# Kernel optimization log

Measured on AMD Instinct MI355X. Metric: run time of the kernel, lower is better.

The kernel has to match this reference:

```python
import jax, jax.numpy as jnp
import numpy as np

NUM_HEADS = 12
HEAD_SIZE = 64
HIDDEN = NUM_HEADS * HEAD_SIZE  # 768
ONE_SIDED_WINDOW = 256          # attention_window 512 // 2
NEG = -10000.0


def setup_inputs() -> dict:
    key = jax.random.key(0)
    ks = jax.random.split(key, 16)
    B, W, E, H = 1, 2048, 128, HIDDEN
    std = 0.02
    def lin(kw, kb):
        return (jax.random.normal(kw, (H, H), jnp.float32) * std,
                jax.random.normal(kb, (H,), jnp.float32) * std)
    q_w, q_b = lin(ks[0], ks[1])
    k_w, k_b = lin(ks[2], ks[3])
    v_w, v_b = lin(ks[4], ks[5])
    w2e_w, w2e_b = lin(ks[6], ks[7])
    e2w_w, e2w_b = lin(ks[8], ks[9])
    e2e_w, e2e_b = lin(ks[10], ks[11])
    return {
        "word_hidden_states": jax.random.normal(ks[12], (B, W, H), jnp.float32),
        "entity_hidden_states": jax.random.normal(ks[13], (B, E, H), jnp.float32),
        "attention_mask": jnp.zeros((B, 1, 1, W + E), jnp.float32),
        "q_w": q_w, "q_b": q_b, "k_w": k_w, "k_b": k_b, "v_w": v_w, "v_b": v_b,
        "w2e_w": w2e_w, "w2e_b": w2e_b, "e2w_w": e2w_w, "e2w_b": e2w_b,
        "e2e_w": e2e_w, "e2e_b": e2e_b,
    }


def reference(word_hidden_states, entity_hidden_states, attention_mask,
              q_w, q_b, k_w, k_b, v_w, v_b,
              w2e_w, w2e_b, e2w_w, e2w_b, e2e_w, e2e_b):
    B, W, H = word_hidden_states.shape
    E = entity_hidden_states.shape[1]
    S = W + E

    def heads(x):  # [B, L, H] -> [B, nh, L, hd]
        return x.reshape(B, -1, NUM_HEADS, HEAD_SIZE).transpose(0, 2, 1, 3)

    concat = jnp.concatenate([word_hidden_states, entity_hidden_states], axis=1)
    k = heads(concat @ k_w + k_b)          # [B, nh, S, hd]
    v = heads(concat @ v_w + v_b)
    q_w2w = heads(word_hidden_states @ q_w + q_b)
    q_w2e = heads(word_hidden_states @ w2e_w + w2e_b)
    q_e2w = heads(entity_hidden_states @ e2w_w + e2w_b)
    q_e2e = heads(entity_hidden_states @ e2e_w + e2e_b)

    k_word, k_ent = k[:, :, :W], k[:, :, W:]

    # --- w2w: Longformer sliding-window QK^T, then _conversion to a dense
    # [B, nh, W, W] matrix with out-of-band entries set to -10000. ---
    w2w = jnp.einsum('bhid,bhjd->bhij', q_w2w, k_word)  # [B, nh, W, W]
    idx = jnp.arange(W)
    in_band = jnp.abs(idx[:, None] - idx[None, :]) <= ONE_SIDED_WINDOW  # [W, W]
    # diagonal mask: float_mask[j] (-10000 where attention_mask != 0) added
    # within the band (broadcast over heads / query positions)
    mask_words = attention_mask[:, 0, 0, :W]                # [B, W]
    float_mask = jnp.where(mask_words != 0.0, NEG, 0.0)     # [B, W]
    w2w = w2w + float_mask[:, None, None, :]
    # _conversion: out-of-band -> -10000; also exact zeros -> -10000 (source quirk)
    w2w = jnp.where(in_band[None, None] & (w2w != 0.0), w2w, NEG)

    # --- entity-aware dense blocks ---
    w2e = jnp.einsum('bhid,bhjd->bhij', q_w2e, k_ent)    # [B, nh, W, E]
    e2w = jnp.einsum('bhid,bhjd->bhij', q_e2w, k_word)   # [B, nh, E, W]
    e2e = jnp.einsum('bhid,bhjd->bhij', q_e2e, k_ent)    # [B, nh, E, E]

    word_scores = jnp.concatenate([w2w, w2e], axis=3)    # [B, nh, W, S]
    ent_scores = jnp.concatenate([e2w, e2e], axis=3)     # [B, nh, E, S]
    scores = jnp.concatenate([word_scores, ent_scores], axis=2)  # [B, nh, S, S]

    scores = scores / jnp.sqrt(jnp.float32(HEAD_SIZE)) + attention_mask
    probs = jax.nn.softmax(scores, axis=-1)

    ctx = jnp.einsum('bhij,bhjd->bhid', probs, v)        # [B, nh, S, hd]
    ctx = ctx.transpose(0, 2, 1, 3).reshape(B, S, H)
    return ctx[:, :W, :], ctx[:, W:, :]
```

## Files before the change

### kernel.cpp

```cpp
#include <hip/hip_runtime.h>

typedef __bf16 bf16x8 __attribute__((ext_vector_type(8)));
typedef unsigned short u16x8 __attribute__((ext_vector_type(8)));
typedef u16x8 u16x8_a __attribute__((may_alias));
typedef unsigned int u32x4 __attribute__((ext_vector_type(4)));
typedef u32x4 u32x4_a __attribute__((may_alias));
typedef float f32x4 __attribute__((ext_vector_type(4)));

#define LOG2E 1.4426950408889634f
#define NEGV  -10000.0f

__device__ __forceinline__ float bf2f(unsigned short u){
  union{unsigned int i; float f;} x; x.i = ((unsigned int)u)<<16; return x.f;
}
__device__ __forceinline__ unsigned short f2bf(float f){
  union{float f; unsigned int i;} x; x.f=f;
  unsigned int i = x.i;
  return (unsigned short)((i + 0x7FFFu + ((i>>16)&1u)) >> 16);
}
__device__ __forceinline__ u16x8 cvt8(float4 a, float4 b){
  u16x8 r;
  r[0]=f2bf(a.x); r[1]=f2bf(a.y); r[2]=f2bf(a.z); r[3]=f2bf(a.w);
  r[4]=f2bf(b.x); r[5]=f2bf(b.y); r[6]=f2bf(b.z); r[7]=f2bf(b.w);
  return r;
}
__device__ __forceinline__ bf16x8 ldb(const unsigned short* p){
  return __builtin_bit_cast(bf16x8, *(const u16x8_a*)p);
}

__global__ __launch_bounds__(256) void transpose6(
    const float* __restrict__ w0, const float* __restrict__ w1,
    const float* __restrict__ w2, const float* __restrict__ w3,
    const float* __restrict__ w4, const float* __restrict__ w5,
    unsigned short* __restrict__ outT)
{
  const float* src;
  switch (blockIdx.z){
    case 0: src = w0; break; case 1: src = w1; break; case 2: src = w2; break;
    case 3: src = w3; break; case 4: src = w4; break; default: src = w5; break;
  }
  unsigned short* dst = outT + (size_t)blockIdx.z * 589824;
  __shared__ float tile[32][33];
  int tx = threadIdx.x, ty = threadIdx.y;
  int x0 = blockIdx.x*32, y0 = blockIdx.y*32;
  #pragma unroll
  for (int i=0;i<32;i+=8) tile[ty+i][tx] = src[(size_t)(y0+ty+i)*768 + x0+tx];
  __syncthreads();
  #pragma unroll
  for (int i=0;i<32;i+=8) dst[(size_t)(x0+ty+i)*768 + y0+tx] = f2bf(tile[tx][ty+i]);
}

__global__ __launch_bounds__(256) void transpose_v(
    const unsigned short* __restrict__ Vb, unsigned short* __restrict__ VbT)
{
  __shared__ unsigned short t[32][33];
  int tx = threadIdx.x, ty = threadIdx.y;
  int x0 = blockIdx.x*32;
  int y0 = blockIdx.y*32;
  #pragma unroll
  for (int i=0;i<32;i+=8) t[ty+i][tx] = Vb[(size_t)(x0+ty+i)*768 + y0+tx];
  __syncthreads();
  #pragma unroll
  for (int i=0;i<32;i+=8) VbT[(size_t)(y0+ty+i)*2176 + x0+tx] = t[tx][ty+i];
}

__global__ __launch_bounds__(256) void gemm_proj(
    const float* __restrict__ word, const float* __restrict__ ent,
    const unsigned short* __restrict__ wT,
    const float* __restrict__ bK, const float* __restrict__ bV,
    const float* __restrict__ bQ, const float* __restrict__ bWE,
    const float* __restrict__ bEW, const float* __restrict__ bEE,
    unsigned short* __restrict__ oK, unsigned short* __restrict__ oV,
    unsigned short* __restrict__ oQ, unsigned short* __restrict__ oWE,
    unsigned short* __restrict__ oEW, unsigned short* __restrict__ oEE)
{
  int mt = blockIdx.x, ntile = blockIdx.y;
  int g, mg;
  if      (mt < 17){ g=0; mg=mt;    }
  else if (mt < 34){ g=1; mg=mt-17; }
  else if (mt < 50){ g=2; mg=mt-34; }
  else if (mt < 66){ g=3; mg=mt-50; }
  else if (mt < 67){ g=4; mg=0;     }
  else             { g=5; mg=0;     }
  int m0 = mg*128;
  const float* A;
  if (g<=1)      A = (mg<16) ? (word + (size_t)m0*768) : ent;
  else if (g<=3) A = word + (size_t)m0*768;
  else           A = ent;
  const unsigned short* B = wT + (size_t)g*589824;
  const float* bias; unsigned short* out;
  switch (g){
    case 0: bias=bK;  out=oK;  break;
    case 1: bias=bV;  out=oV;  break;
    case 2: bias=bQ;  out=oQ;  break;
    case 3: bias=bWE; out=oWE; break;
    case 4: bias=bEW; out=oEW; break;
    default:bias=bEE; out=oEE; break;
  }
  out += (size_t)m0*768;
  int n0 = ntile*128;

  __shared__ __align__(16) unsigned short a_s[128*32];
  __shared__ __align__(16) unsigned short b_s[128*32];

  int tid  = threadIdx.x;
  int w    = tid>>6, lane = tid&63, quad = lane>>4, lr = lane&15;
  int wm   = (w&1)*64, wn = (w>>1)*64;

  f32x4 acc[4][4];
  #pragma unroll
  for (int i=0;i<4;i++) for (int j=0;j<4;j++) for (int r=0;r<4;r++) acc[i][j][r]=0.f;

  int ar = tid>>1;
  int ak = (tid&1)*16;
  const float* Arow = A + (size_t)ar*768 + ak;
  const unsigned short* Brow = B + (size_t)(n0+ar)*768 + ak;

  for (int k0=0; k0<768; k0+=32){
    float4 af0 = *(const float4*)(Arow + k0);
    float4 af1 = *(const float4*)(Arow + k0 + 4);
    float4 af2 = *(const float4*)(Arow + k0 + 8);
    float4 af3 = *(const float4*)(Arow + k0 + 12);
    u16x8 av0 = cvt8(af0, af1);
    u16x8 av1 = cvt8(af2, af3);
    u16x8 bv0 = *(const u16x8_a*)(Brow + k0);
    u16x8 bv1 = *(const u16x8_a*)(Brow + k0 + 8);
    __syncthreads();
    *(u16x8_a*)(a_s + ar*32 + ak)     = av0;
    *(u16x8_a*)(a_s + ar*32 + ak + 8) = av1;
    *(u16x8_a*)(b_s + ar*32 + ak)     = bv0;
    *(u16x8_a*)(b_s + ar*32 + ak + 8) = bv1;
    __syncthreads();
    bf16x8 af[4], bfr[4];
    #pragma unroll
    for (int i=0;i<4;i++) af[i]  = ldb(a_s + (wm+i*16+lr)*32 + quad*8);
    #pragma unroll
    for (int i=0;i<4;i++) bfr[i] = ldb(b_s + (wn+i*16+lr)*32 + quad*8);
    #pragma unroll
    for (int i=0;i<4;i++)
      #pragma unroll
      for (int j=0;j<4;j++)
        acc[i][j] = __builtin_amdgcn_mfma_f32_16x16x32_bf16(af[i], bfr[j], acc[i][j], 0,0,0);
  }
  #pragma unroll
  for (int j=0;j<4;j++){
    int col = n0 + wn + j*16 + lr;
    float bb = bias[col];
    #pragma unroll
    for (int i=0;i<4;i++){
      int rowb = wm + i*16 + quad*4;
      #pragma unroll
      for (int r=0;r<4;r++)
        out[(size_t)(rowb+r)*768 + col] = f2bf(acc[i][j][r] + bb);
    }
  }
}

__global__ __launch_bounds__(256) void attn_split(
  const unsigned short* __restrict__ Kb,  const unsigned short* __restrict__ VbT,
  const unsigned short* __restrict__ Qw,  const unsigned short* __restrict__ Qwe,
  const unsigned short* __restrict__ Qew, const unsigned short* __restrict__ Qee,
  const float* __restrict__ am,
  float* __restrict__ outw, float* __restrict__ oute)
{
  int bx = blockIdx.x, h = blockIdx.y;
  int tid = threadIdx.x, w = tid>>6, lane = tid&63, quad = lane>>4, lr = lane&15;
  bool isword = bx < 64;
  int qrb, kh, nsplit;
  const unsigned short *Qa, *Qb;
  float* outp;
  if (isword){ qrb = bx*32 + (w>>1)*16; kh = w&1; nsplit = 2; Qa=Qw;  Qb=Qwe; outp=outw; }
  else       { qrb = (bx-64)*16;        kh = w;   nsplit = 4; Qa=Qew; Qb=Qee; outp=oute; }

  __shared__ __align__(16) unsigned int p32[4][16*24];
  __shared__ float mrg[4][64][24];

  const unsigned short* qr = Qa + (size_t)(qrb+lr)*768 + h*64 + quad*8;
  bf16x8 qa0 = ldb(qr), qa1 = ldb(qr + 32);
  qr = Qb + (size_t)(qrb+lr)*768 + h*64 + quad*8;
  bf16x8 qb0 = ldb(qr), qb1 = ldb(qr + 32);

  float m_r[4], l_r[4];
  f32x4 o[4];
  #pragma unroll
  for (int r=0;r<4;r++){ m_r[r] = -1e30f; l_r[r] = 0.f; }
  #pragma unroll
  for (int n2=0;n2<4;n2++) for (int r=0;r<4;r++) o[n2][r] = 0.f;

  int lo, nw;
  if (isword){
    lo = qrb - 256; if (lo < 0) lo = 0; lo &= ~31;
    int hi = qrb + 272; if (hi > 2048) hi = 2048; hi = (hi + 31) & ~31;
    nw = (hi - lo) >> 5;
  } else { lo = 0; nw = 64; }
  int nc = nw + 4;

  for (int c = kh; c < nc; c += nsplit){
    bool entp = c >= nw;
    int j0 = entp ? (2048 + (c-nw)*32) : (lo + c*32);

    const unsigned short* kp = Kb + (size_t)(j0+lr)*768 + h*64 + quad*8;
    bf16x8 k00 = ldb(kp),          k01 = ldb(kp + 32);
    bf16x8 k10 = ldb(kp + 16*768), k11 = ldb(kp + 16*768 + 32);
    const unsigned short* vp = VbT + (size_t)(h*64 + lr)*2176 + j0 + quad*8;
    bf16x8 v0 = ldb(vp), v1 = ldb(vp + 16*2176), v2 = ldb(vp + 32*2176), v3 = ldb(vp + 48*2176);

    bf16x8 qf0 = entp ? qb0 : qa0;
    bf16x8 qf1 = entp ? qb1 : qa1;
    f32x4 s[2];
    {
      f32x4 z0 = {0.f,0.f,0.f,0.f}, z1 = {0.f,0.f,0.f,0.f};
      z0 = __builtin_amdgcn_mfma_f32_16x16x32_bf16(qf0, k00, z0, 0,0,0);
      z0 = __builtin_amdgcn_mfma_f32_16x16x32_bf16(qf1, k01, z0, 0,0,0);
      z1 = __builtin_amdgcn_mfma_f32_16x16x32_bf16(qf0, k10, z1, 0,0,0);
      z1 = __builtin_amdgcn_mfma_f32_16x16x32_bf16(qf1, k11, z1, 0,0,0);
      s[0] = z0; s[1] = z1;
    }

    float sc[2][4];
    bool wband = isword && !entp;
    #pragma unroll
    for (int t=0;t<2;t++){
      int j = j0 + t*16 + lr;
      float amj  = am[j];
      float addl = amj * LOG2E;
      #pragma unroll
      for (int r=0;r<4;r++){
        float sv = s[t][r];
        if (wband){
          sv += (amj != 0.f) ? NEGV : 0.f;
          int i = qrb + quad*4 + r;
          bool ok = ((unsigned)(i - j + 256) <= 512u) && (sv != 0.f);
          sv = ok ? sv : NEGV;
        }
        sc[t][r] = sv * (LOG2E*0.125f) + addl;
      }
    }

    #pragma unroll
    for (int r=0;r<4;r++){
      float mx = fmaxf(sc[0][r], sc[1][r]);
      mx = fmaxf(mx, __shfl_xor(mx, 1));
      mx = fmaxf(mx, __shfl_xor(mx, 2));
      mx = fmaxf(mx, __shfl_xor(mx, 4));
      mx = fmaxf(mx, __shfl_xor(mx, 8));
      float mn = fmaxf(m_r[r], mx);
      float alpha = exp2f(m_r[r] - mn);
      m_r[r] = mn;
      float p0 = exp2f(sc[0][r]-mn), p1 = exp2f(sc[1][r]-mn);
      unsigned short pb0 = f2bf(p0), pb1 = f2bf(p1);
      float rs = bf2f(pb0) + bf2f(pb1);
      rs += __shfl_xor(rs,1); rs += __shfl_xor(rs,2);
      rs += __shfl_xor(rs,4); rs += __shfl_xor(rs,8);
      l_r[r] = l_r[r]*alpha + rs;
      p32[w][(quad*4+r)*24 + lr] = (unsigned int)pb0 | ((unsigned int)pb1 << 16);
      #pragma unroll
      for (int n2=0;n2<4;n2++) o[n2][r] *= alpha;
    }

    const unsigned int* pbp = &p32[w][lr*24 + (quad&1)*8];
    u32x4 ra = *(const u32x4_a*)pbp;
    u32x4 rb = *(const u32x4_a*)(pbp + 4);
    unsigned int pf32[4];
    if (quad < 2){
      pf32[0] = (ra[0]&0xFFFFu) | (ra[1]<<16);
      pf32[1] = (ra[2]&0xFFFFu) | (ra[3]<<16);
      pf32[2] = (rb[0]&0xFFFFu) | (rb[1]<<16);
      pf32[3] = (rb[2]&0xFFFFu) | (rb[3]<<16);
    } else {
      pf32[0] = (ra[0]>>16) | (ra[1]&0xFFFF0000u);
      pf32[1] = (ra[2]>>16) | (ra[3]&0xFFFF0000u);
      pf32[2] = (rb[0]>>16) | (rb[1]&0xFFFF0000u);
      pf32[3] = (rb[2]>>16) | (rb[3]&0xFFFF0000u);
    }
    u32x4 pfv = {pf32[0], pf32[1], pf32[2], pf32[3]};
    bf16x8 pf = __builtin_bit_cast(bf16x8, pfv);

    o[0] = __builtin_amdgcn_mfma_f32_16x16x32_bf16(pf, v0, o[0], 0,0,0);
    o[1] = __builtin_amdgcn_mfma_f32_16x16x32_bf16(pf, v1, o[1], 0,0,0);
    o[2] = __builtin_amdgcn_mfma_f32_16x16x32_bf16(pf, v2, o[2], 0,0,0);
    o[3] = __builtin_amdgcn_mfma_f32_16x16x32_bf16(pf, v3, o[3], 0,0,0);
  }

  {
    float* my = &mrg[w][lane][0];
    #pragma unroll
    for (int r=0;r<4;r++){ my[r] = m_r[r]; my[4+r] = l_r[r]; }
    #pragma unroll
    for (int n2=0;n2<4;n2++)
      #pragma unroll
      for (int r=0;r<4;r++) my[8+n2*4+r] = o[n2][r];
  }
  __syncthreads();
  if (kh == 0){
    for (int p=1; p<nsplit; p++){
      const float* pr = &mrg[w+p][lane][0];
      #pragma unroll
      for (int r=0;r<4;r++){
        float m2 = pr[r], l2 = pr[4+r];
        float M  = fmaxf(m_r[r], m2);
        float e1 = exp2f(m_r[r]-M), e2 = exp2f(m2-M);
        m_r[r] = M;
        l_r[r] = l_r[r]*e1 + l2*e2;
        #pragma unroll
        for (int n2=0;n2<4;n2++)
          o[n2][r] = o[n2][r]*e1 + pr[8+n2*4+r]*e2;
      }
    }
    #pragma unroll
    for (int n2=0;n2<4;n2++)
      #pragma unroll
      for (int r=0;r<4;r++){
        int row = qrb + quad*4 + r;
        outp[(size_t)row*768 + h*64 + n2*16 + lr] = o[n2][r] / l_r[r];
      }
  }
}

extern "C" void kernel_launch(void* const* d_in, const int* in_sizes, int n_in,
                              void* d_out, int out_size, void* d_ws, size_t ws_size,
                              hipStream_t stream) {
  const float* word  = (const float*)d_in[0];
  const float* ent   = (const float*)d_in[1];
  const float* am    = (const float*)d_in[2];
  const float* q_w   = (const float*)d_in[3];
  const float* q_b   = (const float*)d_in[4];
  const float* k_w   = (const float*)d_in[5];
  const float* k_b   = (const float*)d_in[6];
  const float* v_w   = (const float*)d_in[7];
  const float* v_b   = (const float*)d_in[8];
  const float* w2e_w = (const float*)d_in[9];
  const float* w2e_b = (const float*)d_in[10];
  const float* e2w_w = (const float*)d_in[11];
  const float* e2w_b = (const float*)d_in[12];
  const float* e2e_w = (const float*)d_in[13];
  const float* e2e_b = (const float*)d_in[14];

  unsigned short* ws  = (unsigned short*)d_ws;
  unsigned short* wT  = ws;
  unsigned short* Kb  = wT  + (size_t)6*589824;
  unsigned short* Vb  = Kb  + (size_t)2176*768;
  unsigned short* Qw  = Vb  + (size_t)2176*768;
  unsigned short* Qwe = Qw  + (size_t)2048*768;
  unsigned short* Qew = Qwe + (size_t)2048*768;
  unsigned short* Qee = Qew + (size_t)128*768;
  unsigned short* VbT = Qee + (size_t)128*768;

  float* outw = (float*)d_out;
  float* oute = outw + (size_t)2048*768;

  hipLaunchKernelGGL(transpose6, dim3(24,24,6), dim3(32,8), 0, stream,
                     k_w, v_w, q_w, w2e_w, e2w_w, e2e_w, wT);
  hipLaunchKernelGGL(gemm_proj, dim3(68,6), dim3(256), 0, stream,
                     word, ent, wT, k_b, v_b, q_b, w2e_b, e2w_b, e2e_b,
                     Kb, Vb, Qw, Qwe, Qew, Qee);
  hipLaunchKernelGGL(transpose_v, dim3(68,24), dim3(32,8), 0, stream, Vb, VbT);
  hipLaunchKernelGGL(attn_split, dim3(72,12), dim3(256), 0, stream,
                     Kb, VbT, Qw, Qwe, Qew, Qee, am, outw, oute);
}
```

Measured before the change: 184.7 us.

## Split attention keys four ways per block and compute row sums via MFMA

Each attention block now handles 16 query rows, with all four waves splitting the key chunks, where before word blocks covered 32 rows with a two-way split. The grid doubles to 136 blocks per head. The softmax row sum now comes from an extra MFMA against a ones vector instead of shuffle reductions, and the final merge is spread so each wave combines and writes one 16-column slice instead of only wave 0 doing it. s_setprio is added around the MFMA groups, and the shared buffers are merged into one region reused for the merge. This raises parallelism and cuts shuffle and merge work, at the cost of loading Q more often and an extra barrier.

```diff
diff --git a/kernel.cpp b/kernel.cpp
--- a/kernel.cpp
+++ b/kernel.cpp
@@ -165,25 +165,31 @@
 {
   int bx = blockIdx.x, h = blockIdx.y;
   int tid = threadIdx.x, w = tid>>6, lane = tid&63, quad = lane>>4, lr = lane&15;
-  bool isword = bx < 64;
-  int qrb, kh, nsplit;
+  bool isword = bx >= 8;
+  int qrb;
   const unsigned short *Qa, *Qb;
   float* outp;
-  if (isword){ qrb = bx*32 + (w>>1)*16; kh = w&1; nsplit = 2; Qa=Qw;  Qb=Qwe; outp=outw; }
-  else       { qrb = (bx-64)*16;        kh = w;   nsplit = 4; Qa=Qew; Qb=Qee; outp=oute; }
-
-  __shared__ __align__(16) unsigned int p32[4][16*24];
-  __shared__ float mrg[4][64][24];
+  if (isword){ qrb = (bx-8)*16; Qa=Qw;  Qb=Qwe; outp=outw; }
+  else       { qrb = bx*16;     Qa=Qew; Qb=Qee; outp=oute; }
+  int kh = w;
+
+  __shared__ __align__(16) unsigned int shb[4*64*24];
+  unsigned int* p32w = shb + w*(16*24);
 
   const unsigned short* qr = Qa + (size_t)(qrb+lr)*768 + h*64 + quad*8;
   bf16x8 qa0 = ldb(qr), qa1 = ldb(qr + 32);
   qr = Qb + (size_t)(qrb+lr)*768 + h*64 + quad*8;
   bf16x8 qb0 = ldb(qr), qb1 = ldb(qr + 32);
 
-  float m_r[4], l_r[4];
-  f32x4 o[4];
-  #pragma unroll
-  for (int r=0;r<4;r++){ m_r[r] = -1e30f; l_r[r] = 0.f; }
+  u16x8 onesu;
+  #pragma unroll
+  for (int i=0;i<8;i++) onesu[i] = 0x3F80;
+  bf16x8 onesf = __builtin_bit_cast(bf16x8, onesu);
+
+  float m_r[4];
+  f32x4 o[4], l4;
+  #pragma unroll
+  for (int r=0;r<4;r++){ m_r[r] = -1e30f; l4[r] = 0.f; }
   #pragma unroll
   for (int n2=0;n2<4;n2++) for (int r=0;r<4;r++) o[n2][r] = 0.f;
 
@@ -195,7 +201,7 @@
   } else { lo = 0; nw = 64; }
   int nc = nw + 4;
 
-  for (int c = kh; c < nc; c += nsplit){
+  for (int c = kh; c < nc; c += 4){
     bool entp = c >= nw;
     int j0 = entp ? (2048 + (c-nw)*32) : (lo + c*32);
 
@@ -210,10 +216,12 @@
     f32x4 s[2];
     {
       f32x4 z0 = {0.f,0.f,0.f,0.f}, z1 = {0.f,0.f,0.f,0.f};
+      __builtin_amdgcn_s_setprio(1);
       z0 = __builtin_amdgcn_mfma_f32_16x16x32_bf16(qf0, k00, z0, 0,0,0);
       z0 = __builtin_amdgcn_mfma_f32_16x16x32_bf16(qf1, k01, z0, 0,0,0);
       z1 = __builtin_amdgcn_mfma_f32_16x16x32_bf16(qf0, k10, z1, 0,0,0);
       z1 = __builtin_amdgcn_mfma_f32_16x16x32_bf16(qf1, k11, z1, 0,0,0);
+      __builtin_amdgcn_s_setprio(0);
       s[0] = z0; s[1] = z1;
     }
 
@@ -249,16 +257,13 @@
       m_r[r] = mn;
       float p0 = exp2f(sc[0][r]-mn), p1 = exp2f(sc[1][r]-mn);
       unsigned short pb0 = f2bf(p0), pb1 = f2bf(p1);
-      float rs = bf2f(pb0) + bf2f(pb1);
-      rs += __shfl_xor(rs,1); rs += __shfl_xor(rs,2);
-      rs += __shfl_xor(rs,4); rs += __shfl_xor(rs,8);
-      l_r[r] = l_r[r]*alpha + rs;
-      p32[w][(quad*4+r)*24 + lr] = (unsigned int)pb0 | ((unsigned int)pb1 << 16);
+      p32w[(quad*4+r)*24 + lr] = (unsigned int)pb0 | ((unsigned int)pb1 << 16);
+      l4[r] *= alpha;
       #pragma unroll
       for (int n2=0;n2<4;n2++) o[n2][r] *= alpha;
     }
 
-    const unsigned int* pbp = &p32[w][lr*24 + (quad&1)*8];
+    const unsigned int* pbp = &p32w[lr*24 + (quad&1)*8];
     u32x4 ra = *(const u32x4_a*)pbp;
     u32x4 rb = *(const u32x4_a*)(pbp + 4);
     unsigned int pf32[4];
@@ -276,44 +281,50 @@
     u32x4 pfv = {pf32[0], pf32[1], pf32[2], pf32[3]};
     bf16x8 pf = __builtin_bit_cast(bf16x8, pfv);
 
+    __builtin_amdgcn_s_setprio(1);
     o[0] = __builtin_amdgcn_mfma_f32_16x16x32_bf16(pf, v0, o[0], 0,0,0);
     o[1] = __builtin_amdgcn_mfma_f32_16x16x32_bf16(pf, v1, o[1], 0,0,0);
     o[2] = __builtin_amdgcn_mfma_f32_16x16x32_bf16(pf, v2, o[2], 0,0,0);
     o[3] = __builtin_amdgcn_mfma_f32_16x16x32_bf16(pf, v3, o[3], 0,0,0);
-  }
-
+    l4   = __builtin_amdgcn_mfma_f32_16x16x32_bf16(pf, onesf, l4, 0,0,0);
+    __builtin_amdgcn_s_setprio(0);
+  }
+
+  __syncthreads();
   {
-    float* my = &mrg[w][lane][0];
-    #pragma unroll
-    for (int r=0;r<4;r++){ my[r] = m_r[r]; my[4+r] = l_r[r]; }
+    float* my = (float*)shb + ((size_t)w*64 + lane)*24;
+    #pragma unroll
+    for (int r=0;r<4;r++){ my[r] = m_r[r]; my[4+r] = l4[r]; }
     #pragma unroll
     for (int n2=0;n2<4;n2++)
       #pragma unroll
       for (int r=0;r<4;r++) my[8+n2*4+r] = o[n2][r];
   }
   __syncthreads();
-  if (kh == 0){
-    for (int p=1; p<nsplit; p++){
-      const float* pr = &mrg[w+p][lane][0];
+  {
+    f32x4 oo = o[w];
+    float mm[4], ll[4];
+    #pragma unroll
+    for (int r=0;r<4;r++){ mm[r] = m_r[r]; ll[r] = l4[r]; }
+    #pragma unroll
+    for (int p=0;p<4;p++){
+      if (p == w) continue;
+      const float* pr = (float*)shb + ((size_t)p*64 + lane)*24;
       #pragma unroll
       for (int r=0;r<4;r++){
-        float m2 = pr[r], l2 = pr[4+r];
-        float M  = fmaxf(m_r[r], m2);
-        float e1 = exp2f(m_r[r]-M), e2 = exp2f(m2-M);
-        m_r[r] = M;
-        l_r[r] = l_r[r]*e1 + l2*e2;
-        #pragma unroll
-        for (int n2=0;n2<4;n2++)
-          o[n2][r] = o[n2][r]*e1 + pr[8+n2*4+r]*e2;
+        float m2 = pr[r], l2 = pr[4+r], o2 = pr[8+w*4+r];
+        float M  = fmaxf(mm[r], m2);
+        float e1 = exp2f(mm[r]-M), e2 = exp2f(m2-M);
+        mm[r] = M;
+        ll[r] = ll[r]*e1 + l2*e2;
+        oo[r] = oo[r]*e1 + o2*e2;
       }
     }
     #pragma unroll
-    for (int n2=0;n2<4;n2++)
-      #pragma unroll
-      for (int r=0;r<4;r++){
-        int row = qrb + quad*4 + r;
-        outp[(size_t)row*768 + h*64 + n2*16 + lr] = o[n2][r] / l_r[r];
-      }
+    for (int r=0;r<4;r++){
+      int row = qrb + quad*4 + r;
+      outp[(size_t)row*768 + h*64 + w*16 + lr] = oo[r] / ll[r];
+    }
   }
 }
 
@@ -355,6 +366,6 @@
                      word, ent, wT, k_b, v_b, q_b, w2e_b, e2w_b, e2e_b,
                      Kb, Vb, Qw, Qwe, Qew, Qee);
   hipLaunchKernelGGL(transpose_v, dim3(68,24), dim3(32,8), 0, stream, Vb, VbT);
-  hipLaunchKernelGGL(attn_split, dim3(72,12), dim3(256), 0, stream,
+  hipLaunchKernelGGL(attn_split, dim3(136,12), dim3(256), 0, stream,
                      Kb, VbT, Qw, Qwe, Qew, Qee, am, outw, oute);
 }
```

Measured after the change: 207.2 us. 12.2% more time.

## Split entity attention rows across two blocks, double-buffer K loads, MFMA row sums

Applied to the files above, without the earlier changes.

Entity query blocks previously walked all 68 key chunks in one block. Their key range is now split in two across twice as many blocks, and a new merge_ent kernel combines the partial outputs using their max and sum statistics. The attention loop prefetches the next K tile while computing the current one, raises wave priority around the MFMAs, and computes row sums with an extra MFMA against a ones vector instead of shuffle reductions. Block IDs are remapped across heads, likely to balance work across XCDs. The cost is an extra kernel launch and partial results written to workspace that reuses the transposed-weight buffer.

```diff
diff --git a/kernel.cpp b/kernel.cpp
--- a/kernel.cpp
+++ b/kernel.cpp
@@ -161,131 +161,166 @@
   const unsigned short* __restrict__ Qw,  const unsigned short* __restrict__ Qwe,
   const unsigned short* __restrict__ Qew, const unsigned short* __restrict__ Qee,
   const float* __restrict__ am,
-  float* __restrict__ outw, float* __restrict__ oute)
+  float* __restrict__ outw, float* __restrict__ pO, float* __restrict__ pML)
 {
-  int bx = blockIdx.x, h = blockIdx.y;
+  int lin = blockIdx.x + 80*blockIdx.y;
+  int wid = (lin & 7)*120 + (lin >> 3);
+  int bx = wid % 80;
+  int h  = wid / 80;
+
   int tid = threadIdx.x, w = tid>>6, lane = tid&63, quad = lane>>4, lr = lane&15;
   bool isword = bx < 64;
-  int qrb, kh, nsplit;
+  int qrb, kh, nsplit, eg=0, ehalf=0;
   const unsigned short *Qa, *Qb;
-  float* outp;
-  if (isword){ qrb = bx*32 + (w>>1)*16; kh = w&1; nsplit = 2; Qa=Qw;  Qb=Qwe; outp=outw; }
-  else       { qrb = (bx-64)*16;        kh = w;   nsplit = 4; Qa=Qew; Qb=Qee; outp=oute; }
+  if (isword){ qrb = bx*32 + (w>>1)*16; kh = w&1; nsplit = 2; Qa=Qw;  Qb=Qwe; }
+  else       { int e = bx-64; eg = e>>1; ehalf = e&1;
+               qrb = eg*16;             kh = w;   nsplit = 4; Qa=Qew; Qb=Qee; }
+  int hofs = h*64;
 
   __shared__ __align__(16) unsigned int p32[4][16*24];
   __shared__ float mrg[4][64][24];
 
-  const unsigned short* qr = Qa + (size_t)(qrb+lr)*768 + h*64 + quad*8;
+  const unsigned short* qr = Qa + (size_t)(qrb+lr)*768 + hofs + quad*8;
   bf16x8 qa0 = ldb(qr), qa1 = ldb(qr + 32);
-  qr = Qb + (size_t)(qrb+lr)*768 + h*64 + quad*8;
+  qr = Qb + (size_t)(qrb+lr)*768 + hofs + quad*8;
   bf16x8 qb0 = ldb(qr), qb1 = ldb(qr + 32);
 
-  float m_r[4], l_r[4];
-  f32x4 o[4];
-  #pragma unroll
-  for (int r=0;r<4;r++){ m_r[r] = -1e30f; l_r[r] = 0.f; }
+  u16x8 onesu;
+  #pragma unroll
+  for (int i=0;i<8;i++) onesu[i] = 0x3F80;
+  bf16x8 onesf = __builtin_bit_cast(bf16x8, onesu);
+
+  unsigned int* p32w = &p32[w][0];
+
+  float m_r[4];
+  f32x4 o[4], l4;
+  #pragma unroll
+  for (int r=0;r<4;r++){ m_r[r] = -1e30f; l4[r] = 0.f; }
   #pragma unroll
   for (int n2=0;n2<4;n2++) for (int r=0;r<4;r++) o[n2][r] = 0.f;
 
-  int lo, nw;
+  int lo, nw, start, end, step;
   if (isword){
     lo = qrb - 256; if (lo < 0) lo = 0; lo &= ~31;
     int hi = qrb + 272; if (hi > 2048) hi = 2048; hi = (hi + 31) & ~31;
     nw = (hi - lo) >> 5;
-  } else { lo = 0; nw = 64; }
-  int nc = nw + 4;
-
-  for (int c = kh; c < nc; c += nsplit){
-    bool entp = c >= nw;
-    int j0 = entp ? (2048 + (c-nw)*32) : (lo + c*32);
-
-    const unsigned short* kp = Kb + (size_t)(j0+lr)*768 + h*64 + quad*8;
-    bf16x8 k00 = ldb(kp),          k01 = ldb(kp + 32);
-    bf16x8 k10 = ldb(kp + 16*768), k11 = ldb(kp + 16*768 + 32);
-    const unsigned short* vp = VbT + (size_t)(h*64 + lr)*2176 + j0 + quad*8;
-    bf16x8 v0 = ldb(vp), v1 = ldb(vp + 16*2176), v2 = ldb(vp + 32*2176), v3 = ldb(vp + 48*2176);
-
-    bf16x8 qf0 = entp ? qb0 : qa0;
-    bf16x8 qf1 = entp ? qb1 : qa1;
-    f32x4 s[2];
-    {
-      f32x4 z0 = {0.f,0.f,0.f,0.f}, z1 = {0.f,0.f,0.f,0.f};
-      z0 = __builtin_amdgcn_mfma_f32_16x16x32_bf16(qf0, k00, z0, 0,0,0);
-      z0 = __builtin_amdgcn_mfma_f32_16x16x32_bf16(qf1, k01, z0, 0,0,0);
-      z1 = __builtin_amdgcn_mfma_f32_16x16x32_bf16(qf0, k10, z1, 0,0,0);
-      z1 = __builtin_amdgcn_mfma_f32_16x16x32_bf16(qf1, k11, z1, 0,0,0);
-      s[0] = z0; s[1] = z1;
+    start = kh; end = nw + 4; step = 2;
+  } else {
+    lo = 0; nw = 64;
+    start = ehalf*34 + kh; end = ehalf*34 + 34; step = 4;
+  }
+
+#define LOADK(K0,K1,K2,K3,CC) do { \
+    bool entp_ = (CC) >= nw; \
+    int j0_ = entp_ ? (2048 + ((CC)-nw)*32) : (lo + (CC)*32); \
+    const unsigned short* kp_ = Kb + (size_t)(j0_+lr)*768 + hofs + quad*8; \
+    K0 = ldb(kp_); K1 = ldb(kp_+32); K2 = ldb(kp_+16*768); K3 = ldb(kp_+16*768+32); \
+  } while(0)
+
+#define COMPUTE(K0,K1,K2,K3,CC) do { \
+    bool entp = (CC) >= nw; \
+    int j0 = entp ? (2048 + ((CC)-nw)*32) : (lo + (CC)*32); \
+    const unsigned short* vp = VbT + (size_t)(hofs + lr)*2176 + j0 + quad*8; \
+    bf16x8 v0 = ldb(vp), v1 = ldb(vp + 16*2176), v2 = ldb(vp + 32*2176), v3 = ldb(vp + 48*2176); \
+    bf16x8 qf0 = entp ? qb0 : qa0; \
+    bf16x8 qf1 = entp ? qb1 : qa1; \
+    f32x4 s[2]; \
+    { \
+      f32x4 z0 = {0.f,0.f,0.f,0.f}, z1 = {0.f,0.f,0.f,0.f}; \
+      __builtin_amdgcn_s_setprio(1); \
+      z0 = __builtin_amdgcn_mfma_f32_16x16x32_bf16(qf0, K0, z0, 0,0,0); \
+      z0 = __builtin_amdgcn_mfma_f32_16x16x32_bf16(qf1, K1, z0, 0,0,0); \
+      z1 = __builtin_amdgcn_mfma_f32_16x16x32_bf16(qf0, K2, z1, 0,0,0); \
+      z1 = __builtin_amdgcn_mfma_f32_16x16x32_bf16(qf1, K3, z1, 0,0,0); \
+      __builtin_amdgcn_s_setprio(0); \
+      s[0] = z0; s[1] = z1; \
+    } \
+    float sc[2][4]; \
+    bool wband = isword && !entp; \
+    _Pragma("unroll") \
+    for (int t=0;t<2;t++){ \
+      int j = j0 + t*16 + lr; \
+      float amj  = am[j]; \
+      float addl = amj * LOG2E; \
+      _Pragma("unroll") \
+      for (int r=0;r<4;r++){ \
+        float sv = s[t][r]; \
+        if (wband){ \
+          sv += (amj != 0.f) ? NEGV : 0.f; \
+          int i = qrb + quad*4 + r; \
+          bool ok = ((unsigned)(i - j + 256) <= 512u) && (sv != 0.f); \
+          sv = ok ? sv : NEGV; \
+        } \
+        sc[t][r] = sv * (LOG2E*0.125f) + addl; \
+      } \
+    } \
+    _Pragma("unroll") \
+    for (int r=0;r<4;r++){ \
+      float mx = fmaxf(sc[0][r], sc[1][r]); \
+      mx = fmaxf(mx, __shfl_xor(mx, 1)); \
+      mx = fmaxf(mx, __shfl_xor(mx, 2)); \
+      mx = fmaxf(mx, __shfl_xor(mx, 4)); \
+      mx = fmaxf(mx, __shfl_xor(mx, 8)); \
+      float mn = fmaxf(m_r[r], mx); \
+      float alpha = exp2f(m_r[r] - mn); \
+      m_r[r] = mn; \
+      float p0 = exp2f(sc[0][r]-mn), p1 = exp2f(sc[1][r]-mn); \
+      unsigned short pb0 = f2bf(p0), pb1 = f2bf(p1); \
+      p32w[(quad*4+r)*24 + lr] = (unsigned int)pb0 | ((unsigned int)pb1 << 16); \
+      l4[r] *= alpha; \
+      _Pragma("unroll") \
+      for (int n2=0;n2<4;n2++) o[n2][r] *= alpha; \
+    } \
+    const unsigned int* pbp = &p32w[lr*24 + (quad&1)*8]; \
+    u32x4 ra = *(const u32x4_a*)pbp; \
+    u32x4 rb = *(const u32x4_a*)(pbp + 4); \
+    unsigned int pf32[4]; \
+    if (quad < 2){ \
+      pf32[0] = (ra[0]&0xFFFFu) | (ra[1]<<16); \
+      pf32[1] = (ra[2]&0xFFFFu) | (ra[3]<<16); \
+      pf32[2] = (rb[0]&0xFFFFu) | (rb[1]<<16); \
+      pf32[3] = (rb[2]&0xFFFFu) | (rb[3]<<16); \
+    } else { \
+      pf32[0] = (ra[0]>>16) | (ra[1]&0xFFFF0000u); \
+      pf32[1] = (ra[2]>>16) | (ra[3]&0xFFFF0000u); \
+      pf32[2] = (rb[0]>>16) | (rb[1]&0xFFFF0000u); \
+      pf32[3] = (rb[2]>>16) | (rb[3]&0xFFFF0000u); \
+    } \
+    u32x4 pfv = {pf32[0], pf32[1], pf32[2], pf32[3]}; \
+    bf16x8 pf = __builtin_bit_cast(bf16x8, pfv); \
+    __builtin_amdgcn_s_setprio(1); \
+    o[0] = __builtin_amdgcn_mfma_f32_16x16x32_bf16(pf, v0, o[0], 0,0,0); \
+    o[1] = __builtin_amdgcn_mfma_f32_16x16x32_bf16(pf, v1, o[1], 0,0,0); \
+    o[2] = __builtin_amdgcn_mfma_f32_16x16x32_bf16(pf, v2, o[2], 0,0,0); \
+    o[3] = __builtin_amdgcn_mfma_f32_16x16x32_bf16(pf, v3, o[3], 0,0,0); \
+    l4   = __builtin_amdgcn_mfma_f32_16x16x32_bf16(pf, onesf, l4, 0,0,0); \
+    __builtin_amdgcn_s_setprio(0); \
+  } while(0)
+
+  {
+    int c = start;
+    bf16x8 kA0,kA1,kA2,kA3, kB0,kB1,kB2,kB3;
+    if (c < end) LOADK(kA0,kA1,kA2,kA3,c);
+    while (c < end) {
+      int c1 = c + step;
+      bool hb = c1 < end;
+      if (hb) LOADK(kB0,kB1,kB2,kB3,c1);
+      COMPUTE(kA0,kA1,kA2,kA3,c);
+      if (!hb) break;
+      int c2 = c1 + step;
+      bool ha = c2 < end;
+      if (ha) LOADK(kA0,kA1,kA2,kA3,c2);
+      COMPUTE(kB0,kB1,kB2,kB3,c1);
+      c = c2;
     }
-
-    float sc[2][4];
-    bool wband = isword && !entp;
-    #pragma unroll
-    for (int t=0;t<2;t++){
-      int j = j0 + t*16 + lr;
-      float amj  = am[j];
-      float addl = amj * LOG2E;
-      #pragma unroll
-      for (int r=0;r<4;r++){
-        float sv = s[t][r];
-        if (wband){
-          sv += (amj != 0.f) ? NEGV : 0.f;
-          int i = qrb + quad*4 + r;
-          bool ok = ((unsigned)(i - j + 256) <= 512u) && (sv != 0.f);
-          sv = ok ? sv : NEGV;
-        }
-        sc[t][r] = sv * (LOG2E*0.125f) + addl;
-      }
-    }
-
-    #pragma unroll
-    for (int r=0;r<4;r++){
-      float mx = fmaxf(sc[0][r], sc[1][r]);
-      mx = fmaxf(mx, __shfl_xor(mx, 1));
-      mx = fmaxf(mx, __shfl_xor(mx, 2));
-      mx = fmaxf(mx, __shfl_xor(mx, 4));
-      mx = fmaxf(mx, __shfl_xor(mx, 8));
-      float mn = fmaxf(m_r[r], mx);
-      float alpha = exp2f(m_r[r] - mn);
-      m_r[r] = mn;
-      float p0 = exp2f(sc[0][r]-mn), p1 = exp2f(sc[1][r]-mn);
-      unsigned short pb0 = f2bf(p0), pb1 = f2bf(p1);
-      float rs = bf2f(pb0) + bf2f(pb1);
-      rs += __shfl_xor(rs,1); rs += __shfl_xor(rs,2);
-      rs += __shfl_xor(rs,4); rs += __shfl_xor(rs,8);
-      l_r[r] = l_r[r]*alpha + rs;
-      p32[w][(quad*4+r)*24 + lr] = (unsigned int)pb0 | ((unsigned int)pb1 << 16);
-      #pragma unroll
-      for (int n2=0;n2<4;n2++) o[n2][r] *= alpha;
-    }
-
-    const unsigned int* pbp = &p32[w][lr*24 + (quad&1)*8];
-    u32x4 ra = *(const u32x4_a*)pbp;
-    u32x4 rb = *(const u32x4_a*)(pbp + 4);
-    unsigned int pf32[4];
-    if (quad < 2){
-      pf32[0] = (ra[0]&0xFFFFu) | (ra[1]<<16);
-      pf32[1] = (ra[2]&0xFFFFu) | (ra[3]<<16);
-      pf32[2] = (rb[0]&0xFFFFu) | (rb[1]<<16);
-      pf32[3] = (rb[2]&0xFFFFu) | (rb[3]<<16);
-    } else {
-      pf32[0] = (ra[0]>>16) | (ra[1]&0xFFFF0000u);
-      pf32[1] = (ra[2]>>16) | (ra[3]&0xFFFF0000u);
-      pf32[2] = (rb[0]>>16) | (rb[1]&0xFFFF0000u);
-      pf32[3] = (rb[2]>>16) | (rb[3]&0xFFFF0000u);
-    }
-    u32x4 pfv = {pf32[0], pf32[1], pf32[2], pf32[3]};
-    bf16x8 pf = __builtin_bit_cast(bf16x8, pfv);
-
-    o[0] = __builtin_amdgcn_mfma_f32_16x16x32_bf16(pf, v0, o[0], 0,0,0);
-    o[1] = __builtin_amdgcn_mfma_f32_16x16x32_bf16(pf, v1, o[1], 0,0,0);
-    o[2] = __builtin_amdgcn_mfma_f32_16x16x32_bf16(pf, v2, o[2], 0,0,0);
-    o[3] = __builtin_amdgcn_mfma_f32_16x16x32_bf16(pf, v3, o[3], 0,0,0);
-  }
+  }
+#undef LOADK
+#undef COMPUTE
 
   {
     float* my = &mrg[w][lane][0];
     #pragma unroll
-    for (int r=0;r<4;r++){ my[r] = m_r[r]; my[4+r] = l_r[r]; }
+    for (int r=0;r<4;r++){ my[r] = m_r[r]; my[4+r] = l4[r]; }
     #pragma unroll
     for (int n2=0;n2<4;n2++)
       #pragma unroll
@@ -301,20 +336,62 @@
         float M  = fmaxf(m_r[r], m2);
         float e1 = exp2f(m_r[r]-M), e2 = exp2f(m2-M);
         m_r[r] = M;
-        l_r[r] = l_r[r]*e1 + l2*e2;
+        l4[r] = l4[r]*e1 + l2*e2;
         #pragma unroll
         for (int n2=0;n2<4;n2++)
           o[n2][r] = o[n2][r]*e1 + pr[8+n2*4+r]*e2;
       }
     }
-    #pragma unroll
-    for (int n2=0;n2<4;n2++)
-      #pragma unroll
-      for (int r=0;r<4;r++){
-        int row = qrb + quad*4 + r;
-        outp[(size_t)row*768 + h*64 + n2*16 + lr] = o[n2][r] / l_r[r];
+    if (isword){
+      #pragma unroll
+      for (int n2=0;n2<4;n2++)
+        #pragma unroll
+        for (int r=0;r<4;r++){
+          int row = qrb + quad*4 + r;
+          outw[(size_t)row*768 + hofs + n2*16 + lr] = o[n2][r] / l4[r];
+        }
+    } else {
+      int idx = (eg*12 + h)*2 + ehalf;
+      float* po = pO + (size_t)idx*1024;
+      #pragma unroll
+      for (int n2=0;n2<4;n2++)
+        #pragma unroll
+        for (int r=0;r<4;r++)
+          po[(quad*4+r)*64 + n2*16 + lr] = o[n2][r];
+      if (lr == 0){
+        float* pml = pML + (size_t)idx*32;
+        #pragma unroll
+        for (int r=0;r<4;r++){
+          pml[(quad*4+r)*2]     = m_r[r];
+          pml[(quad*4+r)*2 + 1] = l4[r];
+        }
       }
-  }
+    }
+  }
+}
+
+__global__ __launch_bounds__(256) void merge_ent(
+    const float* __restrict__ pO, const float* __restrict__ pML,
+    float* __restrict__ oute)
+{
+  int b = blockIdx.x;
+  int g = b/12, h = b%12;
+  int tid = threadIdx.x;
+  int row = tid>>4, cg = tid&15;
+  int i0 = b*2, i1 = b*2+1;
+  float m0 = pML[(size_t)i0*32 + row*2], l0 = pML[(size_t)i0*32 + row*2 + 1];
+  float m1 = pML[(size_t)i1*32 + row*2], l1 = pML[(size_t)i1*32 + row*2 + 1];
+  float M  = fmaxf(m0, m1);
+  float e0 = exp2f(m0-M), e1 = exp2f(m1-M);
+  float rl = 1.f/(l0*e0 + l1*e1);
+  float4 a = *(const float4*)(pO + (size_t)i0*1024 + row*64 + cg*4);
+  float4 c = *(const float4*)(pO + (size_t)i1*1024 + row*64 + cg*4);
+  float4 o;
+  o.x = (a.x*e0 + c.x*e1)*rl;
+  o.y = (a.y*e0 + c.y*e1)*rl;
+  o.z = (a.z*e0 + c.z*e1)*rl;
+  o.w = (a.w*e0 + c.w*e1)*rl;
+  *(float4*)(oute + (size_t)(g*16+row)*768 + h*64 + cg*4) = o;
 }
 
 extern "C" void kernel_launch(void* const* d_in, const int* in_sizes, int n_in,
@@ -346,6 +423,9 @@
   unsigned short* Qee = Qew + (size_t)128*768;
   unsigned short* VbT = Qee + (size_t)128*768;
 
+  float* pO  = (float*)wT;
+  float* pML = pO + (size_t)192*1024;
+
   float* outw = (float*)d_out;
   float* oute = outw + (size_t)2048*768;
 
@@ -355,6 +435,8 @@
                      word, ent, wT, k_b, v_b, q_b, w2e_b, e2w_b, e2e_b,
                      Kb, Vb, Qw, Qwe, Qew, Qee);
   hipLaunchKernelGGL(transpose_v, dim3(68,24), dim3(32,8), 0, stream, Vb, VbT);
-  hipLaunchKernelGGL(attn_split, dim3(72,12), dim3(256), 0, stream,
-                     Kb, VbT, Qw, Qwe, Qew, Qee, am, outw, oute);
-}
+  hipLaunchKernelGGL(attn_split, dim3(80,12), dim3(256), 0, stream,
+                     Kb, VbT, Qw, Qwe, Qew, Qee, am, outw, pO, pML);
+  hipLaunchKernelGGL(merge_ent, dim3(96), dim3(256), 0, stream,
+                     pO, pML, oute);
+}
```

Measured after the change: 192.3 us. 4.1% more time.
